# Kernel tuning notes

Hardware: AMD Instinct MI355X
Metric: run time of the kernel (lower is better)

The kernel has to match this reference:

```python
import jax, jax.numpy as jnp
import numpy as np

L = 512       # seq_len (capped by hard-coded max_length=512)
LEN = 2048    # input feature dim ('length')
D = 2048      # d_model
H = 16        # num_heads
DH = D // H   # d_head = 128
FF = 8192     # FFN hidden
EPS = 1e-5


def _pos_encoding(n, d):
    # Matches PositionalEncoderLayer buffer construction exactly.
    pos = jnp.arange(n, dtype=jnp.float32)[:, None]                              # [n,1]
    freqs = 1.0 / (2.0 * jnp.pi) / (10000.0 * jnp.exp(jnp.arange(0, d, 2, dtype=jnp.float32) / d))
    pe = jnp.zeros((n, d), dtype=jnp.float32)
    pe = pe.at[:, 0::2].set(jnp.sin(2.0 * jnp.pi * freqs * pos))
    pe = pe.at[:, 1::2].set(jnp.cos(2.0 * jnp.pi * freqs * pos))
    return pe


def _layernorm(x, g, b):
    mu = jnp.mean(x, axis=-1, keepdims=True)
    var = jnp.mean((x - mu) ** 2, axis=-1, keepdims=True)
    return (x - mu) / jnp.sqrt(var + EPS) * g + b


def setup_inputs() -> dict:
    key = jax.random.key(0)
    ks = jax.random.split(key, 12)
    def lin(k, fin, fout):
        kw, kb = jax.random.split(k)
        W = jax.random.normal(kw, (fin, fout), jnp.float32) / np.sqrt(fin)
        b = jax.random.normal(kb, (fout,), jnp.float32) * 0.01
        return W, b
    emb_W, emb_b = lin(ks[0], LEN, D)
    Wq, bq = lin(ks[1], D, D)
    Wk, bk = lin(ks[2], D, D)
    Wv, bv = lin(ks[3], D, D)
    Wo, bo = lin(ks[4], D, D)
    W1, b1 = lin(ks[5], D, FF)
    W2, b2 = lin(ks[6], FF, D)
    return {
        "sequence": jax.random.normal(ks[7], (L, LEN), jnp.float32),
        "emb_W": emb_W, "emb_b": emb_b,
        "Wq": Wq, "bq": bq, "Wk": Wk, "bk": bk, "Wv": Wv, "bv": bv,
        "Wo": Wo, "bo": bo,
        "ln_g": jnp.ones((D,), jnp.float32), "ln_b": jnp.zeros((D,), jnp.float32),
        "W1": W1, "b1": b1, "W2": W2, "b2": b2,
    }


def reference(sequence, emb_W, emb_b, Wq, bq, Wk, bk, Wv, bv, Wo, bo, ln_g, ln_b, W1, b1, W2, b2):
    # Embedding + positional encoding
    X = sequence @ emb_W + emb_b                         # [L, D]
    X = X + _pos_encoding(X.shape[0], X.shape[1])
    # Multi-head attention (keeps the module's [L, d_head, H] layout)
    Q = (X @ Wq + bq).reshape(-1, DH, H)
    K = (X @ Wk + bk).reshape(-1, DH, H)
    V = (X @ Wv + bv).reshape(-1, DH, H)
    scores = jnp.einsum('ldh,mdh->lmh', Q, K) / jnp.sqrt(jnp.float32(D))  # [L, L, H]
    attn = jax.nn.softmax(scores, axis=1)                # softmax over keys
    A = jnp.einsum('lmh,mdh->ldh', attn, V).reshape(-1, D) @ Wo + bo
    # Residual + shared LayerNorm, FFN, residual + shared LayerNorm
    Xa = _layernorm(A + X, ln_g, ln_b)
    F = jax.nn.gelu(Xa @ W1 + b1) @ W2 + b2
    return _layernorm(F + Xa, ln_g, ln_b)
```

## Files before the change

### kernel.cpp

```cpp
#include <hip/hip_runtime.h>
#include <hip/hip_bf16.h>


typedef __bf16 bf16_t;
typedef __bf16 bf16x4 __attribute__((ext_vector_type(4)));
typedef __bf16 bf16x8 __attribute__((ext_vector_type(8)));
typedef float  f32x4  __attribute__((ext_vector_type(4)));

#define SEQL 512
#define DM   2048
#define FFH  8192
#define NH   16
#define DHD  128
#define PST  ((size_t)SEQL*DM)

__device__ __forceinline__ unsigned short bfbits(float f){
  bf16_t h = (bf16_t)f;
  return __builtin_bit_cast(unsigned short, h);
}
__device__ __forceinline__ unsigned int pack2(float a, float b){
  return (unsigned int)bfbits(a) | ((unsigned int)bfbits(b) << 16);
}

__device__ __forceinline__ void gll16(const bf16_t* g, bf16_t* l){
  __builtin_amdgcn_global_load_lds(
      (const __attribute__((address_space(1))) void*)g,
      (__attribute__((address_space(3))) void*)l, 16, 0, 0);
}
__device__ __forceinline__ unsigned lds_off(const void* p){
  return (unsigned)(uintptr_t)(const __attribute__((address_space(3))) void*)p;
}

struct CvtSeg { const float* src; bf16_t* dst; int base; };
struct CvtA3  { CvtSeg s[3]; };

template<int NS>
__device__ __forceinline__ void cvt_block8k(const CvtSeg* segs, int b){
  int i = 0;
#pragma unroll
  for (int j = 1; j < NS; ++j) if (b >= segs[j].base) i = j;
  const float* src = segs[i].src;
  bf16_t* dst = segs[i].dst;
  const size_t off0 = (size_t)(b - segs[i].base) * 8192 + threadIdx.x * 8;
  f32x4 v[8];
#pragma unroll
  for (int it = 0; it < 4; ++it){
    v[2*it]   = *(const f32x4*)(src + off0 + it*2048);
    v[2*it+1] = *(const f32x4*)(src + off0 + it*2048 + 4);
  }
#pragma unroll
  for (int it = 0; it < 4; ++it){
    uint4 o;
    o.x = pack2(v[2*it][0],   v[2*it][1]);
    o.y = pack2(v[2*it][2],   v[2*it][3]);
    o.z = pack2(v[2*it+1][0], v[2*it+1][1]);
    o.w = pack2(v[2*it+1][2], v[2*it+1][3]);
    *(uint4*)(dst + off0 + it*2048) = o;
  }
}

template<int NS>
__global__ __launch_bounds__(256)
void cvt8k(CvtA3 a){ cvt_block8k<NS>(a.s, blockIdx.x); }

constexpr int E_PART = 0;
constexpr int E_QKV  = 1;
constexpr int E_FFN1 = 2;

template<int EPI, int PERM, int BM, int NCVT>
__global__ __launch_bounds__(256, (BM == 64) ? 3 : 4)
void gemmT(const bf16_t* __restrict__ A,
           const bf16_t* __restrict__ B0, const bf16_t* __restrict__ B1,
           const bf16_t* __restrict__ B2,
           const float* __restrict__ b0p, const float* __restrict__ b1p,
           const float* __restrict__ b2p,
           float* __restrict__ outF, bf16_t* __restrict__ o0,
           bf16_t* __restrict__ o1, bf16_t* __restrict__ o2,
           int nn, int Nw, int K, int Kc, int gemmN, CvtA3 cva)
{
  if constexpr (NCVT > 0){
    if ((int)blockIdx.x >= gemmN){
      cvt_block8k<NCVT>(cva.s, (int)blockIdx.x - gemmN);
      return;
    }
  }
  constexpr int NF    = (BM == 64) ? 4 : 2;
  constexpr int APASS = BM / 32;
  constexpr int MTM   = (BM == 64) ? 7 : 15;
  constexpr int MTS   = (BM == 64) ? 3 : 4;
  __shared__ bf16_t sA[2][BM*64];
  __shared__ bf16_t sB[2][128*64];
  const int tid  = threadIdx.x;
  const int lane = tid & 63, w = tid >> 6;
  const int wr4 = (BM == 64) ? (w >> 1) : 0;
  const int wc  = (BM == 64) ? (w & 1)  : w;
  const int c = lane & 15, g = lane >> 4;

  const int cpx = gemmN >> 3;
  const int sblk = ((int)blockIdx.x & 7) * cpx + ((int)blockIdx.x >> 3);
  const int mt = sblk & MTM, q2 = sblk >> MTS;
  const int nt = q2 % nn, zt = q2 / nn;
  const int m0 = mt * BM, k0 = zt * Kc;

  const bf16_t* Bsel = B0; int nb0 = nt * 128;
  if constexpr (EPI == E_QKV){
    if (nt >= 32){ Bsel = B2; nb0 = (nt - 32) * 128; }
    else if (nt >= 16){ Bsel = B1; nb0 = (nt - 16) * 128; }
  }

  const int arow = tid >> 3;
  const int acol = (((tid & 7) ^ ((tid >> 3) & 7)) << 3);
  const bf16_t* Aps[APASS];
#pragma unroll
  for (int pa = 0; pa < APASS; ++pa)
    Aps[pa] = A + (size_t)(m0 + pa*32 + arow) * K + k0 + acol;

  const int klB  = (lane >> 3) * 4 + ((lane >> 1) & 3);
  const int colB = nb0 + w*16 + (lane & 1)*8;
  const bf16_t* Bph[2];
  if constexpr (!PERM){
#pragma unroll
    for (int h = 0; h < 2; ++h)
      Bph[h] = Bsel + (size_t)(k0 + h*32 + klB) * Nw + colB;
  }

  const unsigned sBbase[2] = { lds_off(&sB[0][0]), lds_off(&sB[1][0]) };
  const unsigned trLane = (unsigned)(g*256 + c*8);

  f32x4 acc[2][NF] = {};
  const int nk = Kc >> 6;

#define STAGE(bf, kt) {                                                     \
    _Pragma("unroll")                                                       \
    for (int pa = 0; pa < APASS; ++pa)                                      \
      gll16(Aps[pa] + (size_t)(kt)*64, &sA[bf][(pa*256 + tid)*8]);          \
    _Pragma("unroll")                                                       \
    for (int h = 0; h < 2; ++h)                                             \
      _Pragma("unroll")                                                     \
      for (int p = 0; p < 2; ++p){                                          \
        const bf16_t* src;                                                  \
        if constexpr (PERM){                                                \
          const int kr = k0 + (kt)*64 + h*32 + klB;                         \
          const int krow = ((kr & 127) << 4) + (kr >> 7);                   \
          src = Bsel + (size_t)krow * Nw + colB + p*64;                     \
        } else {                                                            \
          src = Bph[h] + (size_t)(kt)*64*Nw + p*64;                         \
        }                                                                   \
        gll16(src, &sB[bf][h*4096 + (p*256 + tid)*8]);                      \
      } }

#define COMPUTE(PB) {                                                       \
    bf16x8 af[2][2]; bf16x8 bq[NF][2];                                      \
    _Pragma("unroll")                                                       \
    for (int m = 0; m < 2; ++m)                                             \
      _Pragma("unroll")                                                     \
      for (int ks = 0; ks < 2; ++ks){                                       \
        const int r = wr4*32 + m*16 + c;                                    \
        af[m][ks] = *(const bf16x8*)&sA[PB][r*64 + (((ks*4+g) ^ (r&7))<<3)];\
      }                                                                     \
    { const unsigned base = sBbase[PB] + (unsigned)(wc*NF*1024) + trLane;   \
      _Pragma("unroll")                                                     \
      for (int n = 0; n < NF; ++n)                                          \
        _Pragma("unroll")                                                   \
        for (int ks = 0; ks < 2; ++ks){                                     \
          bf16x4 r0, r1;                                                    \
          const unsigned a2 = base + (unsigned)(n*1024 + ks*8192);          \
          asm volatile("ds_read_b64_tr_b16 %0, %1" : "=v"(r0) : "v"(a2));   \
          asm volatile("ds_read_b64_tr_b16 %0, %1 offset:128" : "=v"(r1) : "v"(a2)); \
          bq[n][ks] = __builtin_shufflevector(r0, r1, 0,1,2,3,4,5,6,7);     \
        } }                                                                 \
    asm volatile("s_waitcnt lgkmcnt(0)" ::: "memory");                      \
    __builtin_amdgcn_sched_barrier(0);                                      \
    _Pragma("unroll")                                                       \
    for (int m = 0; m < 2; ++m)                                             \
      _Pragma("unroll")                                                     \
      for (int n = 0; n < NF; ++n)                                          \
        _Pragma("unroll")                                                   \
        for (int ks = 0; ks < 2; ++ks)                                      \
          acc[m][n] = __builtin_amdgcn_mfma_f32_16x16x32_bf16(af[m][ks], bq[n][ks], acc[m][n], 0,0,0); }

  STAGE(0, 0);
  asm volatile("s_waitcnt vmcnt(0)" ::: "memory");
  __builtin_amdgcn_s_barrier();
  __builtin_amdgcn_sched_barrier(0);

  int buf = 0;
  for (int kt = 0; kt < nk; ++kt){
    if (kt + 1 < nk){ STAGE(buf ^ 1, kt + 1); }
    COMPUTE(buf);
    asm volatile("s_waitcnt vmcnt(0)" ::: "memory");
    __builtin_amdgcn_s_barrier();
    __builtin_amdgcn_sched_barrier(0);
    buf ^= 1;
  }
#undef STAGE
#undef COMPUTE

#pragma unroll
  for (int n = 0; n < NF; ++n){
    const int col = nt*128 + wc*(NF*16) + n*16 + c;
#pragma unroll
    for (int m = 0; m < 2; ++m){
      const int row0 = m0 + wr4*32 + m*16 + 4*g;
      const f32x4 a4 = acc[m][n];
      if constexpr (EPI == E_PART){
        float* dst = outF + (size_t)zt * PST;
#pragma unroll
        for (int rr = 0; rr < 4; ++rr)
          dst[(size_t)(row0+rr)*DM + col] = a4[rr];
      } else if constexpr (EPI == E_QKV){
        if (col < DM){
          const float bv = b0p[col];
#pragma unroll
          for (int rr = 0; rr < 4; ++rr)
            o0[(size_t)(row0+rr)*DM + col] = (bf16_t)(a4[rr] + bv);
        } else if (col < 2*DM){
          const int cc = col - DM;
          const float bv = b1p[cc];
#pragma unroll
          for (int rr = 0; rr < 4; ++rr)
            o1[(size_t)(row0+rr)*DM + cc] = (bf16_t)(a4[rr] + bv);
        } else {
          const int cc = col - 2*DM;
          const float bv = b2p[cc];
          const int hh = cc & 15, dd = cc >> 4;
          unsigned short us[4];
#pragma unroll
          for (int rr = 0; rr < 4; ++rr) us[rr] = bfbits(a4[rr] + bv);
          *(ushort4*)&o2[(size_t)(hh*DHD + dd)*SEQL + row0] =
              make_ushort4(us[0], us[1], us[2], us[3]);
        }
      } else if constexpr (EPI == E_FFN1){
        const float bv = b0p[col];
#pragma unroll
        for (int rr = 0; rr < 4; ++rr){
          const float v = a4[rr] + bv;
          const float z = v * (v*v*0.044715f + 1.0f) * 1.5957691216f;
          const float gg = v / (1.0f + __expf(-z));
          o0[(size_t)(row0+rr)*FFH + col] = (bf16_t)gg;
        }
      }
    }
  }
}

__global__ __launch_bounds__(256)
void permute_qk(const bf16_t* __restrict__ Qf, const bf16_t* __restrict__ Kf,
                bf16_t* __restrict__ Qhd, bf16_t* __restrict__ Khd)
{
  const int row = blockIdx.x, which = blockIdx.y, tid = threadIdx.x;
  const bf16_t* src = (which ? Kf : Qf) + (size_t)row * DM;
  bf16_t* dst = which ? Khd : Qhd;
  const int hh = tid >> 4, d0 = (tid & 15) * 8;
  unsigned short us[8];
#pragma unroll
  for (int j = 0; j < 8; ++j)
    us[j] = __builtin_bit_cast(unsigned short, src[(d0 + j)*NH + hh]);
  uint4 o;
  o.x = (unsigned)us[0] | ((unsigned)us[1] << 16);
  o.y = (unsigned)us[2] | ((unsigned)us[3] << 16);
  o.z = (unsigned)us[4] | ((unsigned)us[5] << 16);
  o.w = (unsigned)us[6] | ((unsigned)us[7] << 16);
  *(uint4*)&dst[(size_t)hh*(SEQL*DHD) + (size_t)row*DHD + d0] = o;
}

template<int NCVT>
__global__ __launch_bounds__(256)
void attn_cvt(const bf16_t* __restrict__ Qh, const bf16_t* __restrict__ Kh,
              const bf16_t* __restrict__ Vt, bf16_t* __restrict__ Aout,
              int attnN, CvtA3 cva)
{
  if constexpr (NCVT > 0){
    if ((int)blockIdx.x >= attnN){
      cvt_block8k<NCVT>(cva.s, (int)blockIdx.x - attnN);
      return;
    }
  }
  __shared__ bf16_t Pl[32*512];
  __shared__ float redm[4][32];
  __shared__ float reds[4][32];
  const int tid = threadIdx.x;
  const int lane = tid & 63, w = tid >> 6;
  const int c = lane & 15, g = lane >> 4;
  const int h  = (int)blockIdx.x >> 4;
  const int rb = ((int)blockIdx.x & 15) * 32;
  const bf16_t* Qb = Qh + (size_t)h * (SEQL*DHD);
  const bf16_t* Kb = Kh + (size_t)h * (SEQL*DHD);
  const bf16_t* Vb = Vt + (size_t)h * (SEQL*DHD);

  bf16x8 qf[2][4];
#pragma unroll
  for (int a = 0; a < 2; ++a)
#pragma unroll
    for (int ks = 0; ks < 4; ++ks)
      qf[a][ks] = *(const bf16x8*)(Qb + (size_t)(rb + a*16 + c)*DHD + ks*32 + g*8);

  f32x4 s[2][8] = {};
#pragma unroll
  for (int ks = 0; ks < 4; ++ks)
#pragma unroll
    for (int b = 0; b < 8; ++b){
      const bf16x8 kf = *(const bf16x8*)(Kb + (size_t)(w*128 + b*16 + c)*DHD + ks*32 + g*8);
      s[0][b] = __builtin_amdgcn_mfma_f32_16x16x32_bf16(qf[0][ks], kf, s[0][b], 0,0,0);
      s[1][b] = __builtin_amdgcn_mfma_f32_16x16x32_bf16(qf[1][ks], kf, s[1][b], 0,0,0);
    }
#pragma unroll
  for (int a = 0; a < 2; ++a)
#pragma unroll
    for (int b = 0; b < 8; ++b)
#pragma unroll
      for (int rr = 0; rr < 4; ++rr) s[a][b][rr] *= 0.022097086912079612f;

  float mx[2][4], sm[2][4], inv[2][4];
#pragma unroll
  for (int a = 0; a < 2; ++a)
#pragma unroll
    for (int rr = 0; rr < 4; ++rr){
      float m = s[a][0][rr];
#pragma unroll
      for (int b = 1; b < 8; ++b) m = fmaxf(m, s[a][b][rr]);
#pragma unroll
      for (int off = 1; off < 16; off <<= 1) m = fmaxf(m, __shfl_xor(m, off));
      mx[a][rr] = m;
    }
  if (c == 0)
#pragma unroll
    for (int a = 0; a < 2; ++a)
#pragma unroll
      for (int rr = 0; rr < 4; ++rr) redm[w][a*16 + 4*g + rr] = mx[a][rr];
  __syncthreads();
#pragma unroll
  for (int a = 0; a < 2; ++a)
#pragma unroll
    for (int rr = 0; rr < 4; ++rr){
      const int lr = a*16 + 4*g + rr;
      mx[a][rr] = fmaxf(fmaxf(redm[0][lr], redm[1][lr]), fmaxf(redm[2][lr], redm[3][lr]));
      sm[a][rr] = 0.f;
    }
#pragma unroll
  for (int a = 0; a < 2; ++a)
#pragma unroll
    for (int b = 0; b < 8; ++b)
#pragma unroll
      for (int rr = 0; rr < 4; ++rr){
        const float p = __expf(s[a][b][rr] - mx[a][rr]);
        s[a][b][rr] = p;
        sm[a][rr] += p;
      }
#pragma unroll
  for (int a = 0; a < 2; ++a)
#pragma unroll
    for (int rr = 0; rr < 4; ++rr){
#pragma unroll
      for (int off = 1; off < 16; off <<= 1) sm[a][rr] += __shfl_xor(sm[a][rr], off);
    }
  if (c == 0)
#pragma unroll
    for (int a = 0; a < 2; ++a)
#pragma unroll
      for (int rr = 0; rr < 4; ++rr) reds[w][a*16 + 4*g + rr] = sm[a][rr];
  __syncthreads();
#pragma unroll
  for (int a = 0; a < 2; ++a)
#pragma unroll
    for (int rr = 0; rr < 4; ++rr){
      const int lr = a*16 + 4*g + rr;
      inv[a][rr] = 1.0f / (reds[0][lr] + reds[1][lr] + reds[2][lr] + reds[3][lr]);
    }

#pragma unroll
  for (int a = 0; a < 2; ++a)
#pragma unroll
    for (int b = 0; b < 8; ++b)
#pragma unroll
      for (int rr = 0; rr < 4; ++rr){
        const int lr  = a*16 + 4*g + rr;
        const int key = w*128 + b*16 + c;
        const int slot = (key >> 3) ^ (lr & 7);
        Pl[lr*512 + slot*8 + (key & 7)] = (bf16_t)(s[a][b][rr] * inv[a][rr]);
      }
  __syncthreads();

  f32x4 o[2][2] = {};
  const int dw = w * 32;
#pragma unroll
  for (int kst = 0; kst < 16; ++kst){
    bf16x8 pa2[2];
#pragma unroll
    for (int a = 0; a < 2; ++a){
      const int r = a*16 + c;
      const int slot = (kst*4 + g) ^ (r & 7);
      pa2[a] = *(const bf16x8*)&Pl[r*512 + slot*8];
    }
#pragma unroll
    for (int db = 0; db < 2; ++db){
      const bf16x8 vf = *(const bf16x8*)(Vb + (size_t)(dw + db*16 + c)*SEQL + kst*32 + g*8);
      o[0][db] = __builtin_amdgcn_mfma_f32_16x16x32_bf16(pa2[0], vf, o[0][db], 0,0,0);
      o[1][db] = __builtin_amdgcn_mfma_f32_16x16x32_bf16(pa2[1], vf, o[1][db], 0,0,0);
    }
  }
#pragma unroll
  for (int a = 0; a < 2; ++a)
#pragma unroll
    for (int db = 0; db < 2; ++db)
#pragma unroll
      for (int rr = 0; rr < 4; ++rr){
        const int row  = rb + a*16 + 4*g + rr;
        const int col2 = h*DHD + dw + db*16 + c;
        Aout[(size_t)row*DM + col2] = (bf16_t)o[a][db][rr];
      }
}

template<int S>
__global__ __launch_bounds__(256)
void reduce_pos(const float* __restrict__ P, const float* __restrict__ bias,
                float* __restrict__ X, bf16_t* __restrict__ XB)
{
  const int row = blockIdx.x, c0 = threadIdx.x * 8;
  const size_t base = (size_t)row * DM + c0;
  float y[8];
#pragma unroll
  for (int j = 0; j < 8; ++j) y[j] = bias[c0 + j];
#pragma unroll
  for (int s = 0; s < S; ++s){
    const float4 v0 = *(const float4*)(P + s*PST + base);
    const float4 v1 = *(const float4*)(P + s*PST + base + 4);
    y[0]+=v0.x; y[1]+=v0.y; y[2]+=v0.z; y[3]+=v0.w;
    y[4]+=v1.x; y[5]+=v1.y; y[6]+=v1.z; y[7]+=v1.w;
  }
#pragma unroll
  for (int j = 0; j < 8; ++j){
    const int col = c0 + j;
    const float fr  = 1e-4f * __expf(-(float)(col >> 1) * (1.0f/1024.0f));
    const float ang = (float)row * fr;
    y[j] += (col & 1) ? __cosf(ang) : __sinf(ang);
  }
  *(float4*)(X + base)     = make_float4(y[0], y[1], y[2], y[3]);
  *(float4*)(X + base + 4) = make_float4(y[4], y[5], y[6], y[7]);
  uint4 ob;
  ob.x = pack2(y[0], y[1]); ob.y = pack2(y[2], y[3]);
  ob.z = pack2(y[4], y[5]); ob.w = pack2(y[6], y[7]);
  *(uint4*)&XB[base] = ob;
}

template<int S, int WB>
__global__ __launch_bounds__(256)
void reduce_ln(const float* __restrict__ P, const float* __restrict__ bias,
               const float* __restrict__ resid, const float* __restrict__ gam,
               const float* __restrict__ bet, float* __restrict__ outF,
               bf16_t* __restrict__ outB)
{
  const int row = blockIdx.x, tid = threadIdx.x, c0 = tid * 8;
  const size_t base = (size_t)row * DM + c0;
  float y[8];
  {
    const float4 r0 = *(const float4*)(resid + base);
    const float4 r1 = *(const float4*)(resid + base + 4);
    y[0]=r0.x; y[1]=r0.y; y[2]=r0.z; y[3]=r0.w;
    y[4]=r1.x; y[5]=r1.y; y[6]=r1.z; y[7]=r1.w;
  }
#pragma unroll
  for (int j = 0; j < 8; ++j) y[j] += bias[c0 + j];
#pragma unroll
  for (int s = 0; s < S; ++s){
    const float4 v0 = *(const float4*)(P + s*PST + base);
    const float4 v1 = *(const float4*)(P + s*PST + base + 4);
    y[0]+=v0.x; y[1]+=v0.y; y[2]+=v0.z; y[3]+=v0.w;
    y[4]+=v1.x; y[5]+=v1.y; y[6]+=v1.z; y[7]+=v1.w;
  }
  float sm = 0.f, qs = 0.f;
#pragma unroll
  for (int j = 0; j < 8; ++j){ sm += y[j]; qs += y[j]*y[j]; }
#pragma unroll
  for (int off = 32; off >= 1; off >>= 1){
    sm += __shfl_xor(sm, off); qs += __shfl_xor(qs, off);
  }
  __shared__ float rs[4], rq[4];
  const int w = tid >> 6;
  if ((tid & 63) == 0){ rs[w] = sm; rq[w] = qs; }
  __syncthreads();
  sm = rs[0]+rs[1]+rs[2]+rs[3];
  qs = rq[0]+rq[1]+rq[2]+rq[3];
  const float mu   = sm * (1.0f/2048.0f);
  const float var  = qs * (1.0f/2048.0f) - mu*mu;
  const float rstd = rsqrtf(var + 1e-5f);
  const float4 g0 = *(const float4*)(gam + c0);
  const float4 g1 = *(const float4*)(gam + c0 + 4);
  const float4 b0 = *(const float4*)(bet + c0);
  const float4 b1 = *(const float4*)(bet + c0 + 4);
  float o[8];
  o[0] = (y[0]-mu)*rstd*g0.x + b0.x;  o[1] = (y[1]-mu)*rstd*g0.y + b0.y;
  o[2] = (y[2]-mu)*rstd*g0.z + b0.z;  o[3] = (y[3]-mu)*rstd*g0.w + b0.w;
  o[4] = (y[4]-mu)*rstd*g1.x + b1.x;  o[5] = (y[5]-mu)*rstd*g1.y + b1.y;
  o[6] = (y[6]-mu)*rstd*g1.z + b1.z;  o[7] = (y[7]-mu)*rstd*g1.w + b1.w;
  *(float4*)(outF + base)     = make_float4(o[0], o[1], o[2], o[3]);
  *(float4*)(outF + base + 4) = make_float4(o[4], o[5], o[6], o[7]);
  if constexpr (WB){
    uint4 ob;
    ob.x = pack2(o[0], o[1]); ob.y = pack2(o[2], o[3]);
    ob.z = pack2(o[4], o[5]); ob.w = pack2(o[6], o[7]);
    *(uint4*)&outB[base] = ob;
  }
}

extern "C" void kernel_launch(void* const* d_in, const int* in_sizes, int n_in,
                              void* d_out, int out_size, void* d_ws, size_t ws_size,
                              hipStream_t stream)
{
  const float* seq   = (const float*)d_in[0];
  const float* emb_W = (const float*)d_in[1];
  const float* emb_b = (const float*)d_in[2];
  const float* Wq = (const float*)d_in[3];  const float* bq = (const float*)d_in[4];
  const float* Wk = (const float*)d_in[5];  const float* bk = (const float*)d_in[6];
  const float* Wv = (const float*)d_in[7];  const float* bv = (const float*)d_in[8];
  const float* Wo = (const float*)d_in[9];  const float* bo = (const float*)d_in[10];
  const float* ln_g = (const float*)d_in[11]; const float* ln_b = (const float*)d_in[12];
  const float* W1 = (const float*)d_in[13]; const float* b1 = (const float*)d_in[14];
  const float* W2 = (const float*)d_in[15]; const float* b2 = (const float*)d_in[16];

  char* ws = (char*)d_ws;
  size_t off = 0;
  auto take = [&](size_t bytes) -> void* {
    void* p = ws + off;
    off += (bytes + 255) & ~(size_t)255;
    return p;
  };
  bf16_t* seqB = (bf16_t*)take((size_t)SEQL*DM*2);
  bf16_t* WeB  = (bf16_t*)take((size_t)DM*DM*2);
  bf16_t* WqB  = (bf16_t*)take((size_t)DM*DM*2);
  bf16_t* WkB  = (bf16_t*)take((size_t)DM*DM*2);
  bf16_t* WvB  = (bf16_t*)take((size_t)DM*DM*2);
  bf16_t* WoB  = (bf16_t*)take((size_t)DM*DM*2);
  bf16_t* W1B  = (bf16_t*)take((size_t)DM*FFH*2);
  bf16_t* W2B  = (bf16_t*)take((size_t)FFH*DM*2);
  float*  X    = (float*) take((size_t)SEQL*DM*4);
  bf16_t* XB   = (bf16_t*)take((size_t)SEQL*DM*2);
  bf16_t* Qf   = (bf16_t*)take((size_t)SEQL*DM*2);
  bf16_t* Kf   = (bf16_t*)take((size_t)SEQL*DM*2);
  bf16_t* Qhd  = (bf16_t*)take((size_t)SEQL*DM*2);
  bf16_t* Khd  = (bf16_t*)take((size_t)SEQL*DM*2);
  bf16_t* Vt   = (bf16_t*)take((size_t)SEQL*DM*2);
  bf16_t* Afl  = (bf16_t*)take((size_t)SEQL*DM*2);
  float*  Pp   = (float*) take((size_t)8*SEQL*DM*4);
  float*  Xa   = (float*) take((size_t)SEQL*DM*4);
  bf16_t* XaB  = (bf16_t*)take((size_t)SEQL*DM*2);
  bf16_t* Hb   = (bf16_t*)take((size_t)SEQL*FFH*2);
  (void)ws_size; (void)in_sizes; (void)n_in; (void)out_size;

  CvtA3 cz = {};

  CvtA3 c0 = {};
  c0.s[0] = { seq,   seqB, 0 };
  c0.s[1] = { emb_W, WeB,  128 };
  cvt8k<2><<<dim3(640), 256, 0, stream>>>(c0);

  CvtA3 cq = {};
  cq.s[0] = { Wq, WqB, 0 };
  cq.s[1] = { Wk, WkB, 512 };
  cq.s[2] = { Wv, WvB, 1024 };
  gemmT<E_PART,0,64,3><<<dim3(2048), 256, 0, stream>>>(seqB, WeB, nullptr, nullptr,
      nullptr, nullptr, nullptr, Pp, nullptr, nullptr, nullptr, 16, DM, DM, 512, 512, cq);
  reduce_pos<4><<<SEQL, 256, 0, stream>>>(Pp, emb_b, X, XB);

  CvtA3 c1 = {};
  c1.s[0] = { W1, W1B, 0 };
  gemmT<E_QKV,0,32,1><<<dim3(2816), 256, 0, stream>>>(XB, WqB, WkB, WvB,
      bq, bk, bv, nullptr, Qf, Kf, Vt, 48, DM, DM, DM, 768, c1);
  permute_qk<<<dim3(SEQL,2), 256, 0, stream>>>(Qf, Kf, Qhd, Khd);

  CvtA3 c2 = {};
  c2.s[0] = { Wo, WoB, 0 };
  c2.s[1] = { W2, W2B, 512 };
  attn_cvt<2><<<dim3(2816), 256, 0, stream>>>(Qhd, Khd, Vt, Afl, 256, c2);

  gemmT<E_PART,1,64,0><<<dim3(512), 256, 0, stream>>>(Afl, WoB, nullptr, nullptr,
      nullptr, nullptr, nullptr, Pp, nullptr, nullptr, nullptr, 16, DM, DM, 512, 512, cz);
  reduce_ln<4,1><<<SEQL, 256, 0, stream>>>(Pp, bo, X, ln_g, ln_b, Xa, XaB);

  gemmT<E_FFN1,0,32,0><<<dim3(1024), 256, 0, stream>>>(XaB, W1B, nullptr, nullptr,
      b1, nullptr, nullptr, nullptr, Hb, nullptr, nullptr, 64, FFH, DM, DM, 1024, cz);

  gemmT<E_PART,0,64,0><<<dim3(1024), 256, 0, stream>>>(Hb, W2B, nullptr, nullptr,
      nullptr, nullptr, nullptr, Pp, nullptr, nullptr, nullptr, 16, DM, FFH, 1024, 1024, cz);
  reduce_ln<8,0><<<SEQL, 256, 0, stream>>>(Pp, b2, Xa, ln_g, ln_b, (float*)d_out, nullptr);
}
```

Before: 223.5 us.

## Prefetch two K-tiles ahead in GEMM loop and move Wo conversion earlier

```diff
diff --git a/kernel.cpp b/kernel.cpp
--- a/kernel.cpp
+++ b/kernel.cpp
@@ -32,7 +32,7 @@
 }
 
 struct CvtSeg { const float* src; bf16_t* dst; int base; };
-struct CvtA3  { CvtSeg s[3]; };
+struct CvtA4  { CvtSeg s[4]; };
 
 template<int NS>
 __device__ __forceinline__ void cvt_block8k(const CvtSeg* segs, int b){
@@ -61,7 +61,7 @@
 
 template<int NS>
 __global__ __launch_bounds__(256)
-void cvt8k(CvtA3 a){ cvt_block8k<NS>(a.s, blockIdx.x); }
+void cvt8k(CvtA4 a){ cvt_block8k<NS>(a.s, blockIdx.x); }
 
 constexpr int E_PART = 0;
 constexpr int E_QKV  = 1;
@@ -76,7 +76,7 @@
            const float* __restrict__ b2p,
            float* __restrict__ outF, bf16_t* __restrict__ o0,
            bf16_t* __restrict__ o1, bf16_t* __restrict__ o2,
-           int nn, int Nw, int K, int Kc, int gemmN, CvtA3 cva)
+           int nn, int Nw, int K, int Kc, int gemmN, CvtA4 cva)
 {
   if constexpr (NCVT > 0){
     if ((int)blockIdx.x >= gemmN){
@@ -179,22 +179,36 @@
         for (int ks = 0; ks < 2; ++ks)                                      \
           acc[m][n] = __builtin_amdgcn_mfma_f32_16x16x32_bf16(af[m][ks], bq[n][ks], acc[m][n], 0,0,0); }
 
+#define WAIT_NL() {                                                         \
+    if constexpr (BM == 64) asm volatile("s_waitcnt vmcnt(6)" ::: "memory");\
+    else                    asm volatile("s_waitcnt vmcnt(5)" ::: "memory");}
+
   STAGE(0, 0);
-  asm volatile("s_waitcnt vmcnt(0)" ::: "memory");
+  STAGE(1, 1);
+  WAIT_NL();
   __builtin_amdgcn_s_barrier();
   __builtin_amdgcn_sched_barrier(0);
 
   int buf = 0;
   for (int kt = 0; kt < nk; ++kt){
-    if (kt + 1 < nk){ STAGE(buf ^ 1, kt + 1); }
     COMPUTE(buf);
-    asm volatile("s_waitcnt vmcnt(0)" ::: "memory");
     __builtin_amdgcn_s_barrier();
     __builtin_amdgcn_sched_barrier(0);
+    if (kt + 1 < nk){
+      if (kt + 2 < nk){
+        STAGE(buf, kt + 2);
+        WAIT_NL();
+      } else {
+        asm volatile("s_waitcnt vmcnt(0)" ::: "memory");
+      }
+      __builtin_amdgcn_s_barrier();
+      __builtin_amdgcn_sched_barrier(0);
+    }
     buf ^= 1;
   }
 #undef STAGE
 #undef COMPUTE
+#undef WAIT_NL
 
 #pragma unroll
   for (int n = 0; n < NF; ++n){
@@ -268,7 +282,7 @@
 __global__ __launch_bounds__(256)
 void attn_cvt(const bf16_t* __restrict__ Qh, const bf16_t* __restrict__ Kh,
               const bf16_t* __restrict__ Vt, bf16_t* __restrict__ Aout,
-              int attnN, CvtA3 cva)
+              int attnN, CvtA4 cva)
 {
   if constexpr (NCVT > 0){
     if ((int)blockIdx.x >= attnN){
@@ -547,31 +561,31 @@
   bf16_t* Hb   = (bf16_t*)take((size_t)SEQL*FFH*2);
   (void)ws_size; (void)in_sizes; (void)n_in; (void)out_size;
 
-  CvtA3 cz = {};
-
-  CvtA3 c0 = {};
+  CvtA4 cz = {};
+
+  CvtA4 c0 = {};
   c0.s[0] = { seq,   seqB, 0 };
   c0.s[1] = { emb_W, WeB,  128 };
   cvt8k<2><<<dim3(640), 256, 0, stream>>>(c0);
 
-  CvtA3 cq = {};
+  CvtA4 cq = {};
   cq.s[0] = { Wq, WqB, 0 };
   cq.s[1] = { Wk, WkB, 512 };
   cq.s[2] = { Wv, WvB, 1024 };
-  gemmT<E_PART,0,64,3><<<dim3(2048), 256, 0, stream>>>(seqB, WeB, nullptr, nullptr,
+  cq.s[3] = { Wo, WoB, 1536 };
+  gemmT<E_PART,0,64,4><<<dim3(2560), 256, 0, stream>>>(seqB, WeB, nullptr, nullptr,
       nullptr, nullptr, nullptr, Pp, nullptr, nullptr, nullptr, 16, DM, DM, 512, 512, cq);
   reduce_pos<4><<<SEQL, 256, 0, stream>>>(Pp, emb_b, X, XB);
 
-  CvtA3 c1 = {};
+  CvtA4 c1 = {};
   c1.s[0] = { W1, W1B, 0 };
   gemmT<E_QKV,0,32,1><<<dim3(2816), 256, 0, stream>>>(XB, WqB, WkB, WvB,
       bq, bk, bv, nullptr, Qf, Kf, Vt, 48, DM, DM, DM, 768, c1);
   permute_qk<<<dim3(SEQL,2), 256, 0, stream>>>(Qf, Kf, Qhd, Khd);
 
-  CvtA3 c2 = {};
-  c2.s[0] = { Wo, WoB, 0 };
-  c2.s[1] = { W2, W2B, 512 };
-  attn_cvt<2><<<dim3(2816), 256, 0, stream>>>(Qhd, Khd, Vt, Afl, 256, c2);
+  CvtA4 c2 = {};
+  c2.s[0] = { W2, W2B, 0 };
+  attn_cvt<1><<<dim3(2304), 256, 0, stream>>>(Qhd, Khd, Vt, Afl, 256, c2);
 
   gemmT<E_PART,1,64,0><<<dim3(512), 256, 0, stream>>>(Afl, WoB, nullptr, nullptr,
       nullptr, nullptr, nullptr, Pp, nullptr, nullptr, nullptr, 16, DM, DM, 512, 512, cz);
```

Result: no change. 222.6 us (-0.4%).
